# Optimization experiments

Measured on AMD Instinct MI355X. Metric: run time of the kernel, lower is better.

Reference implementation:

```python
import jax, jax.numpy as jnp
import numpy as np
import math

S, B, D, H = 2048, 2, 1024, 16
DK = D // H

def setup_inputs() -> dict:
    key = jax.random.key(0)
    ks = jax.random.split(key, 32)
    f = lambda k, shape, s=1.0: jax.random.normal(k, shape, dtype=jnp.float32) * s
    inp = {
        'qx': f(ks[0], (S, B, D)),
        'kx': f(ks[1], (S, B, D)),
        'vx': f(ks[2], (S, B, D)),
        'qc': f(ks[3], (S, B, D)),
        'kc': f(ks[4], (S, B, D)),
    }
    w = 1.0 / math.sqrt(D)
    names = ['qx_lin', 'kx_lin', 'vx_lin', 'qc_lin', 'kc_lin', 'out_lin']
    for i, n in enumerate(names):
        inp['W_' + n] = f(ks[5 + 2 * i], (D, D), w)
        inp['b_' + n] = f(ks[6 + 2 * i], (D,), w)
    vnames = ['Vqx', 'Vqc', 'Vkx', 'Vkc']
    for i, n in enumerate(vnames):
        inp['W_' + n] = f(ks[17 + 2 * i], (D, 1), w)
        inp['b_' + n] = f(ks[18 + 2 * i], (1,), w)
    return inp

def _forward(qx, kx, vx, qc, kc,
             W_qx_lin, b_qx_lin, W_kx_lin, b_kx_lin, W_vx_lin, b_vx_lin,
             W_qc_lin, b_qc_lin, W_kc_lin, b_kc_lin, W_out_lin, b_out_lin,
             W_Vqx, b_Vqx, W_Vqc, b_Vqc, W_Vkx, b_Vkx, W_Vkc, b_Vkc):
    # [S,B,D] -> [B,S,D]
    qx = jnp.swapaxes(qx, 0, 1)
    kx = jnp.swapaxes(kx, 0, 1)
    vx = jnp.swapaxes(vx, 0, 1)
    qc = jnp.swapaxes(qc, 0, 1)
    kc = jnp.swapaxes(kc, 0, 1)
    bs = qx.shape[0]

    qx = qx @ W_qx_lin + b_qx_lin
    kx = kx @ W_kx_lin + b_kx_lin
    v = vx @ W_vx_lin + b_vx_lin
    qc = qc @ W_qc_lin + b_qc_lin
    kc = kc @ W_kc_lin + b_kc_lin

    lam_q = jax.nn.sigmoid((qx @ W_Vqx + b_Vqx) + (qc @ W_Vqc + b_Vqc))  # [B,S,1]
    lam_k = jax.nn.sigmoid((kx @ W_Vkx + b_Vkx) + (kc @ W_Vkc + b_Vkc))
    q = (1.0 - lam_q) * qx + lam_q * qc
    k = (1.0 - lam_k) * kx + lam_k * kc

    # [B,S,D] -> [B,H,S,dk]
    q = q.reshape(bs, -1, H, DK).transpose(0, 2, 1, 3)
    k = k.reshape(bs, -1, H, DK).transpose(0, 2, 1, 3)
    v = v.reshape(bs, -1, H, DK).transpose(0, 2, 1, 3)

    scores = jnp.einsum('bhqd,bhkd->bhqk', q, k) / math.sqrt(DK)
    attn = jax.nn.softmax(scores, axis=-1)  # dropout is identity in eval
    ctx = jnp.einsum('bhqk,bhkd->bhqd', attn, v)

    concat = ctx.transpose(0, 2, 1, 3).reshape(bs, -1, D)
    out = concat @ W_out_lin + b_out_lin
    return jnp.swapaxes(out, 0, 1)  # back to [S,B,D]

def reference(qx, kx, vx, qc, kc,
              W_qx_lin, b_qx_lin, W_kx_lin, b_kx_lin, W_vx_lin, b_vx_lin,
              W_qc_lin, b_qc_lin, W_kc_lin, b_kc_lin, W_out_lin, b_out_lin,
              W_Vqx, b_Vqx, W_Vqc, b_Vqc, W_Vkx, b_Vkx, W_Vkc, b_Vkc):
    return _forward(qx, kx, vx, qc, kc,
                    W_qx_lin, b_qx_lin, W_kx_lin, b_kx_lin, W_vx_lin, b_vx_lin,
                    W_qc_lin, b_qc_lin, W_kc_lin, b_kc_lin, W_out_lin, b_out_lin,
                    W_Vqx, b_Vqx, W_Vqc, b_Vqc, W_Vkx, b_Vkx, W_Vkc, b_Vkc)
```

## Files before the change

kernel.cpp:

```cpp
#include <hip/hip_runtime.h>
#include <math.h>

typedef unsigned short u16;
typedef __attribute__((ext_vector_type(8))) short short8;
typedef __attribute__((ext_vector_type(4))) float floatx4;
typedef __attribute__((ext_vector_type(4))) unsigned short ushort4v;
typedef __attribute__((ext_vector_type(2))) unsigned int uint2v;

__device__ __forceinline__ float bf2f(u16 x) {
    union { unsigned int u; float f; } v; v.u = ((unsigned int)x) << 16; return v.f;
}
__device__ __forceinline__ u16 f2bf(float f) {
    union { float f; unsigned int u; } v; v.f = f;
    unsigned int r = v.u + 0x7fffu + ((v.u >> 16) & 1u);
    return (u16)(r >> 16);
}
__device__ __forceinline__ unsigned int pk2bf(float a, float b) {
#if __has_builtin(__builtin_amdgcn_cvt_pk_bf16_f32)
    auto r = __builtin_amdgcn_cvt_pk_bf16_f32(a, b);
    union { decltype(r) v; unsigned int u; } cv; cv.v = r; return cv.u;
#else
    return (unsigned int)f2bf(a) | ((unsigned int)f2bf(b) << 16);
#endif
}
__device__ __forceinline__ short8 cvt8(const floatx4 a, const floatx4 b) {
    union { unsigned int u[4]; short8 s; } r;
    r.u[0] = pk2bf(a[0], a[1]); r.u[1] = pk2bf(a[2], a[3]);
    r.u[2] = pk2bf(b[0], b[1]); r.u[3] = pk2bf(b[2], b[3]);
    return r.s;
}

struct WFuseJobs { const float* W[4]; const float* wv[4]; const float* bl[4];
                   float* out[4]; float* bdot; };

__global__ __launch_bounds__(256) void wfuse(WFuseJobs wf) {
    const int z = blockIdx.y;
    const float* W = wf.W[z];
    const float* wv = wf.wv[z];
    float* out = wf.out[z];
    const int t = threadIdx.x;
    const int lane = t & 63, w = t >> 6;
#pragma unroll
    for (int i = 0; i < 4; i++) {
        const int row = blockIdx.x * 16 + w * 4 + i;
        const float* Wr = W + (size_t)row * 1024 + lane * 16;
        const float* vr = wv + lane * 16;
        float p = 0.f;
#pragma unroll
        for (int c = 0; c < 4; c++) {
            const floatx4 a = *(const floatx4*)(Wr + c * 4);
            const floatx4 b = *(const floatx4*)(vr + c * 4);
            p += a[0] * b[0] + a[1] * b[1] + a[2] * b[2] + a[3] * b[3];
        }
#pragma unroll
        for (int m = 1; m <= 32; m <<= 1) p += __shfl_xor(p, m);
        if (lane == 0) out[row] = p;
    }
    if (blockIdx.x == 0) {
        const floatx4 bb = *(const floatx4*)(wf.bl[z] + t * 4);
        const floatx4 vv = *(const floatx4*)(wv + t * 4);
        float p = bb[0] * vv[0] + bb[1] * vv[1] + bb[2] * vv[2] + bb[3] * vv[3];
#pragma unroll
        for (int m = 1; m <= 32; m <<= 1) p += __shfl_xor(p, m);
        __shared__ float red[4];
        if ((t & 63) == 0) red[t >> 6] = p;
        __syncthreads();
        if (t == 0) wf.bdot[z] = red[0] + red[1] + red[2] + red[3];
    }
}

struct DotJobs {
    const float* xa[2]; const float* xc[2];
    const float* w1[2]; const float* w2[2];
    const float* bdot;
    const float* sA[2]; const float* sB[2];
    float* lam[2];
};

__global__ __launch_bounds__(256) void dotk(DotJobs dj) {
    const int z = blockIdx.y;
    const int row = blockIdx.x;
    const int t = threadIdx.x;
    const size_t off = (size_t)row * 1024 + t * 4;
    const floatx4 a  = *(const floatx4*)(dj.xa[z] + off);
    const floatx4 c  = *(const floatx4*)(dj.xc[z] + off);
    const floatx4 w1 = *(const floatx4*)(dj.w1[z] + t * 4);
    const floatx4 w2 = *(const floatx4*)(dj.w2[z] + t * 4);
    float p = 0.f;
#pragma unroll
    for (int j = 0; j < 4; j++) p += a[j] * w1[j] + c[j] * w2[j];
#pragma unroll
    for (int m = 1; m <= 32; m <<= 1) p += __shfl_xor(p, m);
    __shared__ float red[4];
    if ((t & 63) == 0) red[t >> 6] = p;
    __syncthreads();
    if (t == 0) {
        const float x = red[0] + red[1] + red[2] + red[3]
                      + dj.bdot[2 * z] + dj.bdot[2 * z + 1]
                      + dj.sA[z][0] + dj.sB[z][0];
        dj.lam[z][row] = 1.f / (1.f + exp2f(-x * 1.44269504f));
    }
}

struct WTJobs { const float* src[6]; u16* dst[6]; };

__global__ __launch_bounds__(256) void wtrans(WTJobs wj) {
    __shared__ float tile[32][33];
    const int z = blockIdx.z;
    const float* W = wj.src[z];
    u16* Wt = wj.dst[z];
    const int n0 = blockIdx.x * 32, k0 = blockIdx.y * 32;
    const int tx = threadIdx.x & 31, ty = threadIdx.x >> 5;
#pragma unroll
    for (int i = 0; i < 4; i++)
        tile[ty + i * 8][tx] = W[(size_t)(k0 + ty + i * 8) * 1024 + n0 + tx];
    __syncthreads();
#pragma unroll
    for (int i = 0; i < 4; i++)
        Wt[(size_t)(n0 + ty + i * 8) * 1024 + k0 + tx] = f2bf(tile[tx][ty + i * 8]);
}

__global__ __launch_bounds__(256) void vtrans(const u16* __restrict__ V,
                                              u16* __restrict__ Vtg) {
    __shared__ u16 tile[32][34];
    const int bh = blockIdx.z, b = bh >> 4, h = bh & 15;
    const int base = b * 1024 + h * 64;
    const int s0 = blockIdx.x * 32, d0 = blockIdx.y * 32;
    const int tx = threadIdx.x & 31, ty = threadIdx.x >> 5;
#pragma unroll
    for (int i = 0; i < 4; i++)
        tile[ty + i * 8][tx] = V[(size_t)(s0 + ty + i * 8) * 2048 + base + d0 + tx];
    __syncthreads();
#pragma unroll
    for (int i = 0; i < 4; i++)
        Vtg[((size_t)bh * 64 + d0 + ty + i * 8) * 2048 + s0 + tx] = tile[tx][ty + i * 8];
}

struct PJob {
    const float* Aa; const float* Ac; const u16* Ba; const u16* Bc;
    const float* biasA; const float* biasC; const float* lam; u16* out;
};
struct PJobs { PJob j[3]; };

__global__ __launch_bounds__(256, 2) void projall(PJobs jobs) {
    __shared__ u16 Asa[128 * 32];
    __shared__ u16 Asc[128 * 32];
    __shared__ u16 Bsa[128 * 32];
    __shared__ u16 Bsc[128 * 32];
    const PJob jb = jobs.j[blockIdx.z];
    const int K = 1024;
    const int m0 = blockIdx.y * 128;
    const int n0 = blockIdx.x * 128;
    const int t = threadIdx.x;
    const int lane = t & 63;
    const int wid = t >> 6;
    const int wm = wid >> 1, wn = wid & 1;
    const int qd = lane >> 4, lm = lane & 15;

    const int srow = t >> 1, colb = (t & 1) * 16;
    const float* Aap = jb.Aa + (size_t)(m0 + srow) * K + colb;
    const u16*   Bap = jb.Ba + (size_t)(n0 + srow) * K + colb;
    u16* awr  = &Asa[srow * 32 + colb];
    u16* cwr  = &Asc[srow * 32 + colb];
    u16* bawr = &Bsa[srow * 32 + colb];
    u16* bcwr = &Bsc[srow * 32 + colb];

    const floatx4 zero4 = {0.f, 0.f, 0.f, 0.f};

    if (jb.Ac) {
        floatx4 accA[4][4], accC[4][4];
#pragma unroll
        for (int i = 0; i < 4; i++)
#pragma unroll
            for (int j2 = 0; j2 < 4; j2++) { accA[i][j2] = zero4; accC[i][j2] = zero4; }
        const float* Acp = jb.Ac + (size_t)(m0 + srow) * K + colb;
        const u16*   Bcp = jb.Bc + (size_t)(n0 + srow) * K + colb;

        floatx4 pa[4], pc[4];
        short8 pba[2], pbc[2];
#pragma unroll
        for (int q = 0; q < 4; q++) { pa[q] = *(const floatx4*)(Aap + q * 4); pc[q] = *(const floatx4*)(Acp + q * 4); }
        pba[0] = *(const short8*)Bap; pba[1] = *(const short8*)(Bap + 8);
        pbc[0] = *(const short8*)Bcp; pbc[1] = *(const short8*)(Bcp + 8);

        for (int k0 = 0; k0 < K; k0 += 32) {
            __syncthreads();
            *(short8*)awr        = cvt8(pa[0], pa[1]);
            *(short8*)(awr + 8)  = cvt8(pa[2], pa[3]);
            *(short8*)cwr        = cvt8(pc[0], pc[1]);
            *(short8*)(cwr + 8)  = cvt8(pc[2], pc[3]);
            *(short8*)bawr       = pba[0];
            *(short8*)(bawr + 8) = pba[1];
            *(short8*)bcwr       = pbc[0];
            *(short8*)(bcwr + 8) = pbc[1];
            if (k0 + 32 < K) {
                Aap += 32; Acp += 32; Bap += 32; Bcp += 32;
#pragma unroll
                for (int q = 0; q < 4; q++) { pa[q] = *(const floatx4*)(Aap + q * 4); pc[q] = *(const floatx4*)(Acp + q * 4); }
                pba[0] = *(const short8*)Bap; pba[1] = *(const short8*)(Bap + 8);
                pbc[0] = *(const short8*)Bcp; pbc[1] = *(const short8*)(Bcp + 8);
            }
            __syncthreads();

            short8 aa[4], ac[4], ba[4], bc[4];
#pragma unroll
            for (int i = 0; i < 4; i++) {
                aa[i] = *(const short8*)&Asa[(wm * 64 + i * 16 + lm) * 32 + qd * 8];
                ac[i] = *(const short8*)&Asc[(wm * 64 + i * 16 + lm) * 32 + qd * 8];
                ba[i] = *(const short8*)&Bsa[(wn * 64 + i * 16 + lm) * 32 + qd * 8];
                bc[i] = *(const short8*)&Bsc[(wn * 64 + i * 16 + lm) * 32 + qd * 8];
            }
#pragma unroll
            for (int i = 0; i < 4; i++)
#pragma unroll
                for (int j2 = 0; j2 < 4; j2++) {
                    accA[i][j2] = __builtin_amdgcn_mfma_f32_16x16x32_bf16(aa[i], ba[j2], accA[i][j2], 0, 0, 0);
                    accC[i][j2] = __builtin_amdgcn_mfma_f32_16x16x32_bf16(ac[i], bc[j2], accC[i][j2], 0, 0, 0);
                }
        }

#pragma unroll
        for (int i = 0; i < 4; i++) {
            const int mb = m0 + wm * 64 + i * 16 + qd * 4;
            float lamv[4];
#pragma unroll
            for (int r = 0; r < 4; r++) lamv[r] = jb.lam[mb + r];
#pragma unroll
            for (int j2 = 0; j2 < 4; j2++) {
                const int col = n0 + wn * 64 + j2 * 16 + lm;
                const float bA = jb.biasA[col];
                const float bC = jb.biasC[col];
#pragma unroll
                for (int r = 0; r < 4; r++) {
                    const float va = accA[i][j2][r] + bA;
                    const float vc = accC[i][j2][r] + bC;
                    jb.out[(size_t)(mb + r) * 1024 + col] = f2bf(va + lamv[r] * (vc - va));
                }
            }
        }
    } else {
        floatx4 acc[4][4];
#pragma unroll
        for (int i = 0; i < 4; i++)
#pragma unroll
            for (int j2 = 0; j2 < 4; j2++) acc[i][j2] = zero4;

        floatx4 pa[4];
        short8 pba[2];
#pragma unroll
        for (int q = 0; q < 4; q++) pa[q] = *(const floatx4*)(Aap + q * 4);
        pba[0] = *(const short8*)Bap; pba[1] = *(const short8*)(Bap + 8);

        for (int k0 = 0; k0 < K; k0 += 32) {
            __syncthreads();
            *(short8*)awr        = cvt8(pa[0], pa[1]);
            *(short8*)(awr + 8)  = cvt8(pa[2], pa[3]);
            *(short8*)bawr       = pba[0];
            *(short8*)(bawr + 8) = pba[1];
            if (k0 + 32 < K) {
                Aap += 32; Bap += 32;
#pragma unroll
                for (int q = 0; q < 4; q++) pa[q] = *(const floatx4*)(Aap + q * 4);
                pba[0] = *(const short8*)Bap; pba[1] = *(const short8*)(Bap + 8);
            }
            __syncthreads();

            short8 af[4], bfg[4];
#pragma unroll
            for (int i = 0; i < 4; i++) {
                af[i]  = *(const short8*)&Asa[(wm * 64 + i * 16 + lm) * 32 + qd * 8];
                bfg[i] = *(const short8*)&Bsa[(wn * 64 + i * 16 + lm) * 32 + qd * 8];
            }
#pragma unroll
            for (int i = 0; i < 4; i++)
#pragma unroll
                for (int j2 = 0; j2 < 4; j2++)
                    acc[i][j2] = __builtin_amdgcn_mfma_f32_16x16x32_bf16(af[i], bfg[j2], acc[i][j2], 0, 0, 0);
        }

#pragma unroll
        for (int i = 0; i < 4; i++) {
            const int mb = m0 + wm * 64 + i * 16 + qd * 4;
#pragma unroll
            for (int j2 = 0; j2 < 4; j2++) {
                const int col = n0 + wn * 64 + j2 * 16 + lm;
                const float bv = jb.biasA[col];
#pragma unroll
                for (int r = 0; r < 4; r++)
                    jb.out[(size_t)(mb + r) * 1024 + col] = f2bf(acc[i][j2][r] + bv);
            }
        }
    }
}

__global__ __launch_bounds__(256, 4) void gemm64(const u16* __restrict__ A,
                                                 const u16* __restrict__ Bt,
                                                 const float* __restrict__ bias,
                                                 float* __restrict__ C) {
    __shared__ u16 As[64 * 32];
    __shared__ u16 Bs[128 * 32];
    const int K = 1024;
    const int m0 = blockIdx.y * 64;
    const int n0 = blockIdx.x * 128;
    const int t = threadIdx.x;
    const int lane = t & 63;
    const int wid = t >> 6;
    const int wm = wid >> 1, wn = wid & 1;
    const int qd = lane >> 4, lm = lane & 15;

    const floatx4 zero4 = {0.f, 0.f, 0.f, 0.f};
    floatx4 acc[2][4];
#pragma unroll
    for (int i = 0; i < 2; i++)
#pragma unroll
        for (int j2 = 0; j2 < 4; j2++) acc[i][j2] = zero4;

    const int ar = t >> 2, ac_ = (t & 3) * 8;
    const int br = t >> 1, bc_ = (t & 1) * 16;
    const u16* Ap = A + (size_t)(m0 + ar) * K + ac_;
    const u16* Bp = Bt + (size_t)(n0 + br) * K + bc_;
    u16* awr = &As[ar * 32 + ac_];
    u16* bwr = &Bs[br * 32 + bc_];

    short8 pa0, pb0, pb1;
    pa0 = *(const short8*)Ap;
    pb0 = *(const short8*)Bp; pb1 = *(const short8*)(Bp + 8);

    for (int k0 = 0; k0 < K; k0 += 32) {
        __syncthreads();
        *(short8*)awr = pa0;
        *(short8*)bwr = pb0;
        *(short8*)(bwr + 8) = pb1;
        if (k0 + 32 < K) {
            Ap += 32; Bp += 32;
            pa0 = *(const short8*)Ap;
            pb0 = *(const short8*)Bp; pb1 = *(const short8*)(Bp + 8);
        }
        __syncthreads();

        short8 af[2], bfg[4];
#pragma unroll
        for (int i = 0; i < 2; i++)
            af[i] = *(const short8*)&As[(wm * 32 + i * 16 + lm) * 32 + qd * 8];
#pragma unroll
        for (int j2 = 0; j2 < 4; j2++)
            bfg[j2] = *(const short8*)&Bs[(wn * 64 + j2 * 16 + lm) * 32 + qd * 8];
#pragma unroll
        for (int i = 0; i < 2; i++)
#pragma unroll
            for (int j2 = 0; j2 < 4; j2++)
                acc[i][j2] = __builtin_amdgcn_mfma_f32_16x16x32_bf16(af[i], bfg[j2], acc[i][j2], 0, 0, 0);
    }

#pragma unroll
    for (int i = 0; i < 2; i++) {
        const int mb = m0 + wm * 32 + i * 16 + qd * 4;
#pragma unroll
        for (int j2 = 0; j2 < 4; j2++) {
            const int col = n0 + wn * 64 + j2 * 16 + lm;
            const float bv = bias[col];
#pragma unroll
            for (int r = 0; r < 4; r++)
                C[(size_t)(mb + r) * 1024 + col] = acc[i][j2][r] + bv;
        }
    }
}

__global__ __launch_bounds__(256, 2) void attn4(
    const u16* __restrict__ Q, const u16* __restrict__ Kk,
    const u16* __restrict__ Vtg, float* __restrict__ ctxp,
    float* __restrict__ lp) {
    __shared__ u16 Ks[64 * 72];
    __shared__ u16 Vs[64 * 72];
    __shared__ u16 Ps[4 * 64 * 72];

    const int bh = blockIdx.y, b = bh >> 4, h = bh & 15;
    const int sp = blockIdx.z;
    const int base = b * 1024 + h * 64;
    const int t = threadIdx.x, lane = t & 63, w = t >> 6;
    const int qd = lane >> 4, lm = lane & 15;
    const int q0w = blockIdx.x * 256 + w * 64;

    short8 qf[4][2];
#pragma unroll
    for (int qh = 0; qh < 4; qh++) {
        const u16* qr = Q + (size_t)(q0w + qh * 16 + lm) * 2048 + base;
#pragma unroll
        for (int c = 0; c < 2; c++)
            qf[qh][c] = *(const short8*)(qr + c * 32 + qd * 8);
    }

    const floatx4 zero4 = {0.f, 0.f, 0.f, 0.f};
    floatx4 ctx[4][4];
#pragma unroll
    for (int qh = 0; qh < 4; qh++)
#pragma unroll
        for (int g = 0; g < 4; g++) ctx[qh][g] = zero4;
    float lpart[4] = {0.f, 0.f, 0.f, 0.f};

    u16* Pw = &Ps[w * 64 * 72];
    const float C = 0.18033688011112042f;

    const int sr = t >> 3, sc = (t & 7) * 8;
    const u16* ksrc = Kk + (size_t)(sp * 1024 + sr) * 2048 + base + sc;
    const u16* vsrc = Vtg + ((size_t)bh * 64 + sr) * 2048 + sp * 1024 + sc;
    u16* kdst0 = &Ks[sr * 72 + sc];
    u16* kdst1 = &Ks[(sr + 32) * 72 + sc];
    u16* vdst0 = &Vs[sr * 72 + sc];
    u16* vdst1 = &Vs[(sr + 32) * 72 + sc];

    short8 ka0 = *(const short8*)ksrc;
    short8 ka1 = *(const short8*)(ksrc + (size_t)32 * 2048);
    short8 va0 = *(const short8*)vsrc;
    short8 va1 = *(const short8*)(vsrc + (size_t)32 * 2048);

    for (int kt = 0; kt < 16; kt++) {
        __syncthreads();
        *(short8*)kdst0 = ka0;
        *(short8*)kdst1 = ka1;
        *(short8*)vdst0 = va0;
        *(short8*)vdst1 = va1;
        __syncthreads();
        if (kt < 15) {
            ksrc += (size_t)64 * 2048;
            vsrc += 64;
            ka0 = *(const short8*)ksrc;
            ka1 = *(const short8*)(ksrc + (size_t)32 * 2048);
            va0 = *(const short8*)vsrc;
            va1 = *(const short8*)(vsrc + (size_t)32 * 2048);
        }

#pragma unroll
        for (int g = 0; g < 4; g++) {
            const short8 kf0 = *(const short8*)&Ks[(g * 16 + lm) * 72 + qd * 8];
            const short8 kf1 = *(const short8*)&Ks[(g * 16 + lm) * 72 + 32 + qd * 8];
#pragma unroll
            for (int qh = 0; qh < 4; qh++) {
                floatx4 st = zero4;
                st = __builtin_amdgcn_mfma_f32_16x16x32_bf16(kf0, qf[qh][0], st, 0, 0, 0);
                st = __builtin_amdgcn_mfma_f32_16x16x32_bf16(kf1, qf[qh][1], st, 0, 0, 0);
                const float p0 = exp2f(st[0] * C);
                const float p1 = exp2f(st[1] * C);
                const float p2 = exp2f(st[2] * C);
                const float p3 = exp2f(st[3] * C);
                lpart[qh] += (p0 + p1) + (p2 + p3);
                uint2v pw;
                pw[0] = pk2bf(p0, p1);
                pw[1] = pk2bf(p2, p3);
                *(uint2v*)&Pw[(qh * 16 + lm) * 72 + g * 16 + qd * 4] = pw;
            }
        }

        short8 pa[4][2];
#pragma unroll
        for (int qh = 0; qh < 4; qh++)
#pragma unroll
            for (int c = 0; c < 2; c++)
                pa[qh][c] = *(const short8*)&Pw[(qh * 16 + lm) * 72 + c * 32 + qd * 8];
#pragma unroll
        for (int g = 0; g < 4; g++) {
            const short8 vb0 = *(const short8*)&Vs[(g * 16 + lm) * 72 + qd * 8];
            const short8 vb1 = *(const short8*)&Vs[(g * 16 + lm) * 72 + 32 + qd * 8];
#pragma unroll
            for (int qh = 0; qh < 4; qh++) {
                ctx[qh][g] = __builtin_amdgcn_mfma_f32_16x16x32_bf16(pa[qh][0], vb0, ctx[qh][g], 0, 0, 0);
                ctx[qh][g] = __builtin_amdgcn_mfma_f32_16x16x32_bf16(pa[qh][1], vb1, ctx[qh][g], 0, 0, 0);
            }
        }
    }

    float* cbase = ctxp + (size_t)sp * 4194304;
#pragma unroll
    for (int qh = 0; qh < 4; qh++) {
        float l = lpart[qh];
        l += __shfl_xor(l, 16);
        l += __shfl_xor(l, 32);
        if (lane < 16)
            lp[(size_t)sp * 65536 + bh * 2048 + q0w + qh * 16 + lane] = l;
#pragma unroll
        for (int r = 0; r < 4; r++) {
            const int srow = q0w + qh * 16 + qd * 4 + r;
            float* orow = cbase + (size_t)srow * 2048 + base;
#pragma unroll
            for (int g = 0; g < 4; g++)
                orow[g * 16 + lm] = ctx[qh][g][r];
        }
    }
}

__global__ __launch_bounds__(256) void merge(const float* __restrict__ ctxp,
                                             const float* __restrict__ lp,
                                             u16* __restrict__ out) {
    const size_t idx = ((size_t)blockIdx.x * 256 + threadIdx.x) * 4;
    const floatx4 a = *(const floatx4*)(ctxp + idx);
    const floatx4 c = *(const floatx4*)(ctxp + 4194304 + idx);
    const int srow = (int)(idx >> 11);
    const int rem = (int)(idx & 2047);
    const int bh = rem >> 6;
    const float l = lp[bh * 2048 + srow] + lp[65536 + bh * 2048 + srow];
    const float inv = 1.0f / l;
    ushort4v o;
    const unsigned int lo = pk2bf((a[0] + c[0]) * inv, (a[1] + c[1]) * inv);
    const unsigned int hi = pk2bf((a[2] + c[2]) * inv, (a[3] + c[3]) * inv);
    o[0] = (u16)(lo & 0xffff); o[1] = (u16)(lo >> 16);
    o[2] = (u16)(hi & 0xffff); o[3] = (u16)(hi >> 16);
    *(ushort4v*)(out + idx) = o;
}

extern "C" void kernel_launch(void* const* d_in, const int* in_sizes, int n_in,
                              void* d_out, int out_size, void* d_ws, size_t ws_size,
                              hipStream_t stream) {
    const float* qx = (const float*)d_in[0];
    const float* kx = (const float*)d_in[1];
    const float* vx = (const float*)d_in[2];
    const float* qc = (const float*)d_in[3];
    const float* kc = (const float*)d_in[4];
    const float* W_qx = (const float*)d_in[5];   const float* b_qx = (const float*)d_in[6];
    const float* W_kx = (const float*)d_in[7];   const float* b_kx = (const float*)d_in[8];
    const float* W_vx = (const float*)d_in[9];   const float* b_vx = (const float*)d_in[10];
    const float* W_qc = (const float*)d_in[11];  const float* b_qc = (const float*)d_in[12];
    const float* W_kc = (const float*)d_in[13];  const float* b_kc = (const float*)d_in[14];
    const float* W_out = (const float*)d_in[15]; const float* b_out = (const float*)d_in[16];
    const float* W_Vqx = (const float*)d_in[17]; const float* b_Vqx = (const float*)d_in[18];
    const float* W_Vqc = (const float*)d_in[19]; const float* b_Vqc = (const float*)d_in[20];
    const float* W_Vkx = (const float*)d_in[21]; const float* b_Vkx = (const float*)d_in[22];
    const float* W_Vkc = (const float*)d_in[23]; const float* b_Vkc = (const float*)d_in[24];

    char* ws = (char*)d_ws;
    const size_t MB = 1048576;
    float* ctxp = (float*)ws;
    u16* Vtg    = (u16*)(ws + 32 * MB);
    u16* Wt[6];
    for (int i = 0; i < 6; i++) Wt[i] = (u16*)(ws + 40 * MB + (size_t)i * 2 * MB);
    u16* Pv    = (u16*)(ws + 52 * MB);
    u16* qg    = (u16*)(ws + 60 * MB);
    u16* kg    = (u16*)(ws + 68 * MB);
    u16* ctxbf = (u16*)(ws + 76 * MB);
    float* wfused = (float*)(ws + 84 * MB);
    float* bdot   = (float*)(ws + 84 * MB + 16384);
    float* lam    = (float*)(ws + 84 * MB + 16384 + 256);
    float* l_part = (float*)(ws + 84 * MB + 16384 + 256 + 32768);

    WFuseJobs wf;
    wf.W[0] = W_qx; wf.wv[0] = W_Vqx; wf.bl[0] = b_qx; wf.out[0] = wfused;
    wf.W[1] = W_qc; wf.wv[1] = W_Vqc; wf.bl[1] = b_qc; wf.out[1] = wfused + 1024;
    wf.W[2] = W_kx; wf.wv[2] = W_Vkx; wf.bl[2] = b_kx; wf.out[2] = wfused + 2048;
    wf.W[3] = W_kc; wf.wv[3] = W_Vkc; wf.bl[3] = b_kc; wf.out[3] = wfused + 3072;
    wf.bdot = bdot;
    wfuse<<<dim3(64, 4), 256, 0, stream>>>(wf);

    DotJobs dj;
    dj.xa[0] = qx; dj.xc[0] = qc; dj.w1[0] = wfused;        dj.w2[0] = wfused + 1024;
    dj.sA[0] = b_Vqx; dj.sB[0] = b_Vqc; dj.lam[0] = lam;
    dj.xa[1] = kx; dj.xc[1] = kc; dj.w1[1] = wfused + 2048; dj.w2[1] = wfused + 3072;
    dj.sA[1] = b_Vkx; dj.sB[1] = b_Vkc; dj.lam[1] = lam + 4096;
    dj.bdot = bdot;
    dotk<<<dim3(4096, 2), 256, 0, stream>>>(dj);

    WTJobs wj;
    const float* wsrc[6] = {W_qx, W_kx, W_vx, W_qc, W_kc, W_out};
    for (int i = 0; i < 6; i++) { wj.src[i] = wsrc[i]; wj.dst[i] = Wt[i]; }
    wtrans<<<dim3(32, 32, 6), 256, 0, stream>>>(wj);

    PJobs pj;
    pj.j[0].Aa = qx; pj.j[0].Ac = qc; pj.j[0].Ba = Wt[0]; pj.j[0].Bc = Wt[3];
    pj.j[0].biasA = b_qx; pj.j[0].biasC = b_qc; pj.j[0].lam = lam;        pj.j[0].out = qg;
    pj.j[1].Aa = kx; pj.j[1].Ac = kc; pj.j[1].Ba = Wt[1]; pj.j[1].Bc = Wt[4];
    pj.j[1].biasA = b_kx; pj.j[1].biasC = b_kc; pj.j[1].lam = lam + 4096; pj.j[1].out = kg;
    pj.j[2].Aa = vx; pj.j[2].Ac = nullptr; pj.j[2].Ba = Wt[2]; pj.j[2].Bc = nullptr;
    pj.j[2].biasA = b_vx; pj.j[2].biasC = nullptr; pj.j[2].lam = nullptr; pj.j[2].out = Pv;
    projall<<<dim3(8, 32, 3), 256, 0, stream>>>(pj);

    vtrans<<<dim3(64, 2, 32), 256, 0, stream>>>(Pv, Vtg);

    attn4<<<dim3(8, 32, 2), 256, 0, stream>>>(qg, kg, Vtg, ctxp, l_part);

    merge<<<4096, 256, 0, stream>>>(ctxp, l_part, ctxbf);

    gemm64<<<dim3(8, 64), 256, 0, stream>>>(ctxbf, Wt[5], b_out, (float*)d_out);
}
```

Before: 380.5 us.

## Pre-scale gated inputs into bf16 and fuse dual projections into one K=2048 GEMM

The gating kernel now computes lambda, then writes bf16 copies of (1-lambda)*x and lambda*c side by side, and also casts v to bf16. The transposed weights are stacked so the q and k projections become single GEMMs with K=2048 over bf16 inputs, with the bias blend applied in the epilogue. This removes the in-GEMM fp32 loads and conversions and the doubled accumulators, allowing higher occupancy. The cost is an extra bf16 intermediate written and read through memory.

```diff
diff --git a/kernel.cpp b/kernel.cpp
--- a/kernel.cpp
+++ b/kernel.cpp
@@ -23,12 +23,6 @@
     return (unsigned int)f2bf(a) | ((unsigned int)f2bf(b) << 16);
 #endif
 }
-__device__ __forceinline__ short8 cvt8(const floatx4 a, const floatx4 b) {
-    union { unsigned int u[4]; short8 s; } r;
-    r.u[0] = pk2bf(a[0], a[1]); r.u[1] = pk2bf(a[2], a[3]);
-    r.u[2] = pk2bf(b[0], b[1]); r.u[3] = pk2bf(b[2], b[3]);
-    return r.s;
-}
 
 struct WFuseJobs { const float* W[4]; const float* wv[4]; const float* bl[4];
                    float* out[4]; float* bdot; };
@@ -69,23 +63,35 @@
     }
 }
 
-struct DotJobs {
-    const float* xa[2]; const float* xc[2];
-    const float* w1[2]; const float* w2[2];
+struct GCJobs {
+    const float* xa[3]; const float* xc[3];
+    const float* w1[3]; const float* w2[3];
     const float* bdot;
-    const float* sA[2]; const float* sB[2];
-    float* lam[2];
+    const float* sA[3]; const float* sB[3];
+    float* lamout[3];
+    u16* dst[3];
 };
 
-__global__ __launch_bounds__(256) void dotk(DotJobs dj) {
+__global__ __launch_bounds__(256) void gatecast(GCJobs gj) {
     const int z = blockIdx.y;
     const int row = blockIdx.x;
     const int t = threadIdx.x;
     const size_t off = (size_t)row * 1024 + t * 4;
-    const floatx4 a  = *(const floatx4*)(dj.xa[z] + off);
-    const floatx4 c  = *(const floatx4*)(dj.xc[z] + off);
-    const floatx4 w1 = *(const floatx4*)(dj.w1[z] + t * 4);
-    const floatx4 w2 = *(const floatx4*)(dj.w2[z] + t * 4);
+    const floatx4 a = *(const floatx4*)(gj.xa[z] + off);
+
+    if (z == 2) {
+        ushort4v o;
+        const unsigned int lo = pk2bf(a[0], a[1]);
+        const unsigned int hi = pk2bf(a[2], a[3]);
+        o[0] = (u16)(lo & 0xffff); o[1] = (u16)(lo >> 16);
+        o[2] = (u16)(hi & 0xffff); o[3] = (u16)(hi >> 16);
+        *(ushort4v*)(gj.dst[2] + (size_t)row * 1024 + t * 4) = o;
+        return;
+    }
+
+    const floatx4 c  = *(const floatx4*)(gj.xc[z] + off);
+    const floatx4 w1 = *(const floatx4*)(gj.w1[z] + t * 4);
+    const floatx4 w2 = *(const floatx4*)(gj.w2[z] + t * 4);
     float p = 0.f;
 #pragma unroll
     for (int j = 0; j < 4; j++) p += a[j] * w1[j] + c[j] * w2[j];
@@ -94,21 +100,39 @@
     __shared__ float red[4];
     if ((t & 63) == 0) red[t >> 6] = p;
     __syncthreads();
-    if (t == 0) {
-        const float x = red[0] + red[1] + red[2] + red[3]
-                      + dj.bdot[2 * z] + dj.bdot[2 * z + 1]
-                      + dj.sA[z][0] + dj.sB[z][0];
-        dj.lam[z][row] = 1.f / (1.f + exp2f(-x * 1.44269504f));
-    }
-}
-
-struct WTJobs { const float* src[6]; u16* dst[6]; };
+    const float x = red[0] + red[1] + red[2] + red[3]
+                  + gj.bdot[2 * z] + gj.bdot[2 * z + 1]
+                  + gj.sA[z][0] + gj.sB[z][0];
+    const float lam = 1.f / (1.f + exp2f(-x * 1.44269504f));
+    if (t == 0) gj.lamout[z][row] = lam;
+    const float oml = 1.f - lam;
+
+    u16* d = gj.dst[z] + (size_t)row * 2048 + t * 4;
+    ushort4v o1, o2;
+    {
+        const unsigned int lo = pk2bf(oml * a[0], oml * a[1]);
+        const unsigned int hi = pk2bf(oml * a[2], oml * a[3]);
+        o1[0] = (u16)(lo & 0xffff); o1[1] = (u16)(lo >> 16);
+        o1[2] = (u16)(hi & 0xffff); o1[3] = (u16)(hi >> 16);
+    }
+    {
+        const unsigned int lo = pk2bf(lam * c[0], lam * c[1]);
+        const unsigned int hi = pk2bf(lam * c[2], lam * c[3]);
+        o2[0] = (u16)(lo & 0xffff); o2[1] = (u16)(lo >> 16);
+        o2[2] = (u16)(hi & 0xffff); o2[3] = (u16)(hi >> 16);
+    }
+    *(ushort4v*)d = o1;
+    *(ushort4v*)(d + 1024) = o2;
+}
+
+struct WTJobs { const float* src[6]; u16* dst[6]; int stride[6]; int koff[6]; };
 
 __global__ __launch_bounds__(256) void wtrans(WTJobs wj) {
     __shared__ float tile[32][33];
     const int z = blockIdx.z;
     const float* W = wj.src[z];
     u16* Wt = wj.dst[z];
+    const int stride = wj.stride[z], koff = wj.koff[z];
     const int n0 = blockIdx.x * 32, k0 = blockIdx.y * 32;
     const int tx = threadIdx.x & 31, ty = threadIdx.x >> 5;
 #pragma unroll
@@ -117,7 +141,7 @@
     __syncthreads();
 #pragma unroll
     for (int i = 0; i < 4; i++)
-        Wt[(size_t)(n0 + ty + i * 8) * 1024 + k0 + tx] = f2bf(tile[tx][ty + i * 8]);
+        Wt[(size_t)(n0 + ty + i * 8) * stride + koff + k0 + tx] = f2bf(tile[tx][ty + i * 8]);
 }
 
 __global__ __launch_bounds__(256) void vtrans(const u16* __restrict__ V,
@@ -137,18 +161,16 @@
 }
 
 struct PJob {
-    const float* Aa; const float* Ac; const u16* Ba; const u16* Bc;
+    const u16* A; const u16* Bt; int K;
     const float* biasA; const float* biasC; const float* lam; u16* out;
 };
 struct PJobs { PJob j[3]; };
 
-__global__ __launch_bounds__(256, 2) void projall(PJobs jobs) {
-    __shared__ u16 Asa[128 * 32];
-    __shared__ u16 Asc[128 * 32];
-    __shared__ u16 Bsa[128 * 32];
-    __shared__ u16 Bsc[128 * 32];
+__global__ __launch_bounds__(256, 3) void projall(PJobs jobs) {
+    __shared__ u16 As[128 * 32];
+    __shared__ u16 Bs[128 * 32];
     const PJob jb = jobs.j[blockIdx.z];
-    const int K = 1024;
+    const int K = jb.K;
     const int m0 = blockIdx.y * 128;
     const int n0 = blockIdx.x * 128;
     const int t = threadIdx.x;
@@ -157,137 +179,73 @@
     const int wm = wid >> 1, wn = wid & 1;
     const int qd = lane >> 4, lm = lane & 15;
 
+    const floatx4 zero4 = {0.f, 0.f, 0.f, 0.f};
+    floatx4 acc[4][4];
+#pragma unroll
+    for (int i = 0; i < 4; i++)
+#pragma unroll
+        for (int j2 = 0; j2 < 4; j2++) acc[i][j2] = zero4;
+
     const int srow = t >> 1, colb = (t & 1) * 16;
-    const float* Aap = jb.Aa + (size_t)(m0 + srow) * K + colb;
-    const u16*   Bap = jb.Ba + (size_t)(n0 + srow) * K + colb;
-    u16* awr  = &Asa[srow * 32 + colb];
-    u16* cwr  = &Asc[srow * 32 + colb];
-    u16* bawr = &Bsa[srow * 32 + colb];
-    u16* bcwr = &Bsc[srow * 32 + colb];
-
-    const floatx4 zero4 = {0.f, 0.f, 0.f, 0.f};
-
-    if (jb.Ac) {
-        floatx4 accA[4][4], accC[4][4];
+    const u16* Ap = jb.A + (size_t)(m0 + srow) * K + colb;
+    const u16* Bp = jb.Bt + (size_t)(n0 + srow) * K + colb;
+    u16* awr = &As[srow * 32 + colb];
+    u16* bwr = &Bs[srow * 32 + colb];
+
+    short8 pa0 = *(const short8*)Ap;
+    short8 pa1 = *(const short8*)(Ap + 8);
+    short8 pb0 = *(const short8*)Bp;
+    short8 pb1 = *(const short8*)(Bp + 8);
+
+    for (int k0 = 0; k0 < K; k0 += 32) {
+        __syncthreads();
+        *(short8*)awr       = pa0;
+        *(short8*)(awr + 8) = pa1;
+        *(short8*)bwr       = pb0;
+        *(short8*)(bwr + 8) = pb1;
+        if (k0 + 32 < K) {
+            Ap += 32; Bp += 32;
+            pa0 = *(const short8*)Ap;
+            pa1 = *(const short8*)(Ap + 8);
+            pb0 = *(const short8*)Bp;
+            pb1 = *(const short8*)(Bp + 8);
+        }
+        __syncthreads();
+
+        short8 af[4], bfg[4];
+#pragma unroll
+        for (int i = 0; i < 4; i++) {
+            af[i]  = *(const short8*)&As[(wm * 64 + i * 16 + lm) * 32 + qd * 8];
+            bfg[i] = *(const short8*)&Bs[(wn * 64 + i * 16 + lm) * 32 + qd * 8];
+        }
 #pragma unroll
         for (int i = 0; i < 4; i++)
 #pragma unroll
-            for (int j2 = 0; j2 < 4; j2++) { accA[i][j2] = zero4; accC[i][j2] = zero4; }
-        const float* Acp = jb.Ac + (size_t)(m0 + srow) * K + colb;
-        const u16*   Bcp = jb.Bc + (size_t)(n0 + srow) * K + colb;
-
-        floatx4 pa[4], pc[4];
-        short8 pba[2], pbc[2];
-#pragma unroll
-        for (int q = 0; q < 4; q++) { pa[q] = *(const floatx4*)(Aap + q * 4); pc[q] = *(const floatx4*)(Acp + q * 4); }
-        pba[0] = *(const short8*)Bap; pba[1] = *(const short8*)(Bap + 8);
-        pbc[0] = *(const short8*)Bcp; pbc[1] = *(const short8*)(Bcp + 8);
-
-        for (int k0 = 0; k0 < K; k0 += 32) {
-            __syncthreads();
-            *(short8*)awr        = cvt8(pa[0], pa[1]);
-            *(short8*)(awr + 8)  = cvt8(pa[2], pa[3]);
-            *(short8*)cwr        = cvt8(pc[0], pc[1]);
-            *(short8*)(cwr + 8)  = cvt8(pc[2], pc[3]);
-            *(short8*)bawr       = pba[0];
-            *(short8*)(bawr + 8) = pba[1];
-            *(short8*)bcwr       = pbc[0];
-            *(short8*)(bcwr + 8) = pbc[1];
-            if (k0 + 32 < K) {
-                Aap += 32; Acp += 32; Bap += 32; Bcp += 32;
-#pragma unroll
-                for (int q = 0; q < 4; q++) { pa[q] = *(const floatx4*)(Aap + q * 4); pc[q] = *(const floatx4*)(Acp + q * 4); }
-                pba[0] = *(const short8*)Bap; pba[1] = *(const short8*)(Bap + 8);
-                pbc[0] = *(const short8*)Bcp; pbc[1] = *(const short8*)(Bcp + 8);
-            }
-            __syncthreads();
-
-            short8 aa[4], ac[4], ba[4], bc[4];
-#pragma unroll
-            for (int i = 0; i < 4; i++) {
-                aa[i] = *(const short8*)&Asa[(wm * 64 + i * 16 + lm) * 32 + qd * 8];
-                ac[i] = *(const short8*)&Asc[(wm * 64 + i * 16 + lm) * 32 + qd * 8];
-                ba[i] = *(const short8*)&Bsa[(wn * 64 + i * 16 + lm) * 32 + qd * 8];
-                bc[i] = *(const short8*)&Bsc[(wn * 64 + i * 16 + lm) * 32 + qd * 8];
-            }
-#pragma unroll
-            for (int i = 0; i < 4; i++)
-#pragma unroll
-                for (int j2 = 0; j2 < 4; j2++) {
-                    accA[i][j2] = __builtin_amdgcn_mfma_f32_16x16x32_bf16(aa[i], ba[j2], accA[i][j2], 0, 0, 0);
-                    accC[i][j2] = __builtin_amdgcn_mfma_f32_16x16x32_bf16(ac[i], bc[j2], accC[i][j2], 0, 0, 0);
-                }
-        }
-
-#pragma unroll
-        for (int i = 0; i < 4; i++) {
-            const int mb = m0 + wm * 64 + i * 16 + qd * 4;
-            float lamv[4];
+            for (int j2 = 0; j2 < 4; j2++)
+                acc[i][j2] = __builtin_amdgcn_mfma_f32_16x16x32_bf16(af[i], bfg[j2], acc[i][j2], 0, 0, 0);
+    }
+
+#pragma unroll
+    for (int i = 0; i < 4; i++) {
+        const int mb = m0 + wm * 64 + i * 16 + qd * 4;
+        float lamv[4];
+        if (jb.lam) {
 #pragma unroll
             for (int r = 0; r < 4; r++) lamv[r] = jb.lam[mb + r];
-#pragma unroll
-            for (int j2 = 0; j2 < 4; j2++) {
-                const int col = n0 + wn * 64 + j2 * 16 + lm;
-                const float bA = jb.biasA[col];
-                const float bC = jb.biasC[col];
-#pragma unroll
-                for (int r = 0; r < 4; r++) {
-                    const float va = accA[i][j2][r] + bA;
-                    const float vc = accC[i][j2][r] + bC;
-                    jb.out[(size_t)(mb + r) * 1024 + col] = f2bf(va + lamv[r] * (vc - va));
-                }
-            }
-        }
-    } else {
-        floatx4 acc[4][4];
-#pragma unroll
-        for (int i = 0; i < 4; i++)
-#pragma unroll
-            for (int j2 = 0; j2 < 4; j2++) acc[i][j2] = zero4;
-
-        floatx4 pa[4];
-        short8 pba[2];
-#pragma unroll
-        for (int q = 0; q < 4; q++) pa[q] = *(const floatx4*)(Aap + q * 4);
-        pba[0] = *(const short8*)Bap; pba[1] = *(const short8*)(Bap + 8);
-
-        for (int k0 = 0; k0 < K; k0 += 32) {
-            __syncthreads();
-            *(short8*)awr        = cvt8(pa[0], pa[1]);
-            *(short8*)(awr + 8)  = cvt8(pa[2], pa[3]);
-            *(short8*)bawr       = pba[0];
-            *(short8*)(bawr + 8) = pba[1];
-            if (k0 + 32 < K) {
-                Aap += 32; Bap += 32;
-#pragma unroll
-                for (int q = 0; q < 4; q++) pa[q] = *(const floatx4*)(Aap + q * 4);
-                pba[0] = *(const short8*)Bap; pba[1] = *(const short8*)(Bap + 8);
-            }
-            __syncthreads();
-
-            short8 af[4], bfg[4];
-#pragma unroll
-            for (int i = 0; i < 4; i++) {
-                af[i]  = *(const short8*)&Asa[(wm * 64 + i * 16 + lm) * 32 + qd * 8];
-                bfg[i] = *(const short8*)&Bsa[(wn * 64 + i * 16 + lm) * 32 + qd * 8];
-            }
-#pragma unroll
-            for (int i = 0; i < 4; i++)
-#pragma unroll
-                for (int j2 = 0; j2 < 4; j2++)
-                    acc[i][j2] = __builtin_amdgcn_mfma_f32_16x16x32_bf16(af[i], bfg[j2], acc[i][j2], 0, 0, 0);
-        }
-
-#pragma unroll
-        for (int i = 0; i < 4; i++) {
-            const int mb = m0 + wm * 64 + i * 16 + qd * 4;
-#pragma unroll
-            for (int j2 = 0; j2 < 4; j2++) {
-                const int col = n0 + wn * 64 + j2 * 16 + lm;
-                const float bv = jb.biasA[col];
+        }
+#pragma unroll
+        for (int j2 = 0; j2 < 4; j2++) {
+            const int col = n0 + wn * 64 + j2 * 16 + lm;
+            const float bA = jb.biasA[col];
+            if (jb.lam) {
+                const float dB = jb.biasC[col] - bA;
 #pragma unroll
                 for (int r = 0; r < 4; r++)
-                    jb.out[(size_t)(mb + r) * 1024 + col] = f2bf(acc[i][j2][r] + bv);
+                    jb.out[(size_t)(mb + r) * 1024 + col] = f2bf(acc[i][j2][r] + bA + lamv[r] * dB);
+            } else {
+#pragma unroll
+                for (int r = 0; r < 4; r++)
+                    jb.out[(size_t)(mb + r) * 1024 + col] = f2bf(acc[i][j2][r] + bA);
             }
         }
     }
@@ -528,10 +486,13 @@
 
     char* ws = (char*)d_ws;
     const size_t MB = 1048576;
-    float* ctxp = (float*)ws;
-    u16* Vtg    = (u16*)(ws + 32 * MB);
-    u16* Wt[6];
-    for (int i = 0; i < 6; i++) Wt[i] = (u16*)(ws + 40 * MB + (size_t)i * 2 * MB);
+    u16* Aq  = (u16*)ws;
+    u16* Ak  = (u16*)(ws + 16 * MB);
+    u16* Av  = (u16*)(ws + 32 * MB);
+    u16* Wtq = (u16*)(ws + 40 * MB);
+    u16* Wtk = (u16*)(ws + 44 * MB);
+    u16* Wtv = (u16*)(ws + 48 * MB);
+    u16* Wto = (u16*)(ws + 50 * MB);
     u16* Pv    = (u16*)(ws + 52 * MB);
     u16* qg    = (u16*)(ws + 60 * MB);
     u16* kg    = (u16*)(ws + 68 * MB);
@@ -540,6 +501,8 @@
     float* bdot   = (float*)(ws + 84 * MB + 16384);
     float* lam    = (float*)(ws + 84 * MB + 16384 + 256);
     float* l_part = (float*)(ws + 84 * MB + 16384 + 256 + 32768);
+    float* ctxp = (float*)ws;
+    u16* Vtg    = (u16*)(ws + 32 * MB);
 
     WFuseJobs wf;
     wf.W[0] = W_qx; wf.wv[0] = W_Vqx; wf.bl[0] = b_qx; wf.out[0] = wfused;
@@ -549,25 +512,31 @@
     wf.bdot = bdot;
     wfuse<<<dim3(64, 4), 256, 0, stream>>>(wf);
 
-    DotJobs dj;
-    dj.xa[0] = qx; dj.xc[0] = qc; dj.w1[0] = wfused;        dj.w2[0] = wfused + 1024;
-    dj.sA[0] = b_Vqx; dj.sB[0] = b_Vqc; dj.lam[0] = lam;
-    dj.xa[1] = kx; dj.xc[1] = kc; dj.w1[1] = wfused + 2048; dj.w2[1] = wfused + 3072;
-    dj.sA[1] = b_Vkx; dj.sB[1] = b_Vkc; dj.lam[1] = lam + 4096;
-    dj.bdot = bdot;
-    dotk<<<dim3(4096, 2), 256, 0, stream>>>(dj);
+    GCJobs gj;
+    gj.xa[0] = qx; gj.xc[0] = qc; gj.w1[0] = wfused;        gj.w2[0] = wfused + 1024;
+    gj.sA[0] = b_Vqx; gj.sB[0] = b_Vqc; gj.lamout[0] = lam;        gj.dst[0] = Aq;
+    gj.xa[1] = kx; gj.xc[1] = kc; gj.w1[1] = wfused + 2048; gj.w2[1] = wfused + 3072;
+    gj.sA[1] = b_Vkx; gj.sB[1] = b_Vkc; gj.lamout[1] = lam + 4096; gj.dst[1] = Ak;
+    gj.xa[2] = vx; gj.xc[2] = nullptr; gj.w1[2] = nullptr; gj.w2[2] = nullptr;
+    gj.sA[2] = nullptr; gj.sB[2] = nullptr; gj.lamout[2] = nullptr; gj.dst[2] = Av;
+    gj.bdot = bdot;
+    gatecast<<<dim3(4096, 3), 256, 0, stream>>>(gj);
 
     WTJobs wj;
-    const float* wsrc[6] = {W_qx, W_kx, W_vx, W_qc, W_kc, W_out};
-    for (int i = 0; i < 6; i++) { wj.src[i] = wsrc[i]; wj.dst[i] = Wt[i]; }
+    wj.src[0] = W_qx; wj.dst[0] = Wtq; wj.stride[0] = 2048; wj.koff[0] = 0;
+    wj.src[1] = W_qc; wj.dst[1] = Wtq; wj.stride[1] = 2048; wj.koff[1] = 1024;
+    wj.src[2] = W_kx; wj.dst[2] = Wtk; wj.stride[2] = 2048; wj.koff[2] = 0;
+    wj.src[3] = W_kc; wj.dst[3] = Wtk; wj.stride[3] = 2048; wj.koff[3] = 1024;
+    wj.src[4] = W_vx; wj.dst[4] = Wtv; wj.stride[4] = 1024; wj.koff[4] = 0;
+    wj.src[5] = W_out; wj.dst[5] = Wto; wj.stride[5] = 1024; wj.koff[5] = 0;
     wtrans<<<dim3(32, 32, 6), 256, 0, stream>>>(wj);
 
     PJobs pj;
-    pj.j[0].Aa = qx; pj.j[0].Ac = qc; pj.j[0].Ba = Wt[0]; pj.j[0].Bc = Wt[3];
+    pj.j[0].A = Aq; pj.j[0].Bt = Wtq; pj.j[0].K = 2048;
     pj.j[0].biasA = b_qx; pj.j[0].biasC = b_qc; pj.j[0].lam = lam;        pj.j[0].out = qg;
-    pj.j[1].Aa = kx; pj.j[1].Ac = kc; pj.j[1].Ba = Wt[1]; pj.j[1].Bc = Wt[4];
+    pj.j[1].A = Ak; pj.j[1].Bt = Wtk; pj.j[1].K = 2048;
     pj.j[1].biasA = b_kx; pj.j[1].biasC = b_kc; pj.j[1].lam = lam + 4096; pj.j[1].out = kg;
-    pj.j[2].Aa = vx; pj.j[2].Ac = nullptr; pj.j[2].Ba = Wt[2]; pj.j[2].Bc = nullptr;
+    pj.j[2].A = Av; pj.j[2].Bt = Wtv; pj.j[2].K = 1024;
     pj.j[2].biasA = b_vx; pj.j[2].biasC = nullptr; pj.j[2].lam = nullptr; pj.j[2].out = Pv;
     projall<<<dim3(8, 32, 3), 256, 0, stream>>>(pj);
 
@@ -577,5 +546,5 @@
 
     merge<<<4096, 256, 0, stream>>>(ctxp, l_part, ctxbf);
 
-    gemm64<<<dim3(8, 64), 256, 0, stream>>>(ctxbf, Wt[5], b_out, (float*)d_out);
-}
+    gemm64<<<dim3(8, 64), 256, 0, stream>>>(ctxbf, Wto, b_out, (float*)d_out);
+}
```

After: 351.8 us. -7.5%, faster.
